# Optimization experiments

Measured on AMD Instinct MI355X. Metric: run time of the kernel, lower is better.

The kernel has to match this reference:

```python
import jax, jax.numpy as jnp
import numpy as np

EMBED_DIM = 1024
NUM_HEADS = 16
HEAD_DIM = EMBED_DIM // NUM_HEADS


def setup_inputs() -> dict:
    key = jax.random.key(0)
    k1, k2, k3, k4 = jax.random.split(key, 4)
    B, S, D = 2, 2048, EMBED_DIM
    x = jax.random.normal(k1, (B, S, D), dtype=jnp.float32)
    xpos = jax.random.randint(k2, (B, S), 0, 2048, dtype=jnp.int32)
    # torch nn.Linear weights: [out_features, in_features]; qkv_bias=False -> no qkv bias
    qkv_w = jax.random.normal(k3, (3 * D, D), dtype=jnp.float32) * (D ** -0.5)
    proj_w = jax.random.normal(k4, (D, D), dtype=jnp.float32) * (D ** -0.5)
    proj_b = jnp.zeros((D,), dtype=jnp.float32)
    return {"x": x, "xpos": xpos, "qkv_w": qkv_w, "proj_w": proj_w, "proj_b": proj_b}


def reference(x, xpos, qkv_w, proj_w, proj_b):
    # rope is None, dropout rates are 0, so xpos is unused and dropout is identity.
    B, S, D = x.shape
    H, hd = NUM_HEADS, D // NUM_HEADS
    scale = hd ** -0.5

    qkv = x @ qkv_w.T                                   # [B, S, 3D]
    qkv = qkv.reshape(B, S, 3, H, hd)
    qkv = jnp.transpose(qkv, (0, 3, 2, 1, 4))           # [B, H, 3, S, hd]
    q, k, v = qkv[:, :, 0], qkv[:, :, 1], qkv[:, :, 2]  # each [B, H, S, hd]

    scores = jnp.einsum("bhqd,bhkd->bhqk", q, k) * scale  # [B, H, S, S]
    probs = jax.nn.softmax(scores, axis=-1)
    out = jnp.einsum("bhqk,bhkd->bhqd", probs, v)         # [B, H, S, hd]

    out = jnp.transpose(out, (0, 2, 1, 3)).reshape(B, S, D)
    out = out @ proj_w.T + proj_b
    return out
```

## Files before the change

kernel.cpp:

```cpp
#include <hip/hip_runtime.h>


typedef __bf16 bf16_8 __attribute__((ext_vector_type(8)));
typedef __bf16 bf16_4 __attribute__((ext_vector_type(4)));
typedef __bf16 bf16_2 __attribute__((ext_vector_type(2)));
typedef float floatx4 __attribute__((ext_vector_type(4)));

#define MFMA16 __builtin_amdgcn_mfma_f32_16x16x32_bf16
#define CSCALE 0.1803368801111204f
#define EXP2R  __builtin_amdgcn_exp2f

__device__ __forceinline__ void gld16(const __bf16* g, __bf16* l) {
    __builtin_amdgcn_global_load_lds(
        (const __attribute__((address_space(1))) void*)g,
        (__attribute__((address_space(3))) void*)l, 16, 0, 0);
}

__device__ __forceinline__ unsigned pk_bf16(float a, float b) {
    bf16_2 t;
    t[0] = (__bf16)a; t[1] = (__bf16)b;
    return __builtin_bit_cast(unsigned, t);
}

__global__ __launch_bounds__(256) void cvt_all(
    const float* __restrict__ x, const float* __restrict__ w1,
    const float* __restrict__ w2,
    __bf16* __restrict__ xb, __bf16* __restrict__ w1b, __bf16* __restrict__ w2b)
{
    const int i = blockIdx.x * 256 + threadIdx.x;
    const float* src; __bf16* dst; int off;
    if (i < (1 << 20))                  { src = x;  dst = xb;  off = i; }
    else if (i < (1 << 20) + 786432)    { src = w1; dst = w1b; off = i - (1 << 20); }
    else                                { src = w2; dst = w2b; off = i - (1 << 20) - 786432; }
    float4 v = ((const float4*)src)[off];
    bf16_4 o;
    o[0] = (__bf16)v.x; o[1] = (__bf16)v.y; o[2] = (__bf16)v.z; o[3] = (__bf16)v.w;
    ((bf16_4*)dst)[off] = o;
}

__global__ __launch_bounds__(512) void qkv_gemm(
    const __bf16* __restrict__ X, const __bf16* __restrict__ W,
    __bf16* __restrict__ q_ws, __bf16* __restrict__ k_ws, __bf16* __restrict__ vt_ws)
{
    __shared__ __align__(16) __bf16 S[2][2][128 * 64];

    const int tid = threadIdx.x, lane = tid & 63;
    const int half = tid >> 8, htid = tid & 255;
    const int wvh = (tid >> 6) & 3;
    const int quad = lane >> 4, l15 = lane & 15;
    const int wm = (wvh >> 1) * 64, wn = (wvh & 1) * 64;
    const int m0 = blockIdx.y * 128, n0 = blockIdx.x * 128;
    const int c = n0 >> 10;

    const __bf16* Abase;
    const __bf16* Bbase;
    if (c == 2) { Abase = X + (size_t)m0 * 1024; Bbase = W + (size_t)n0 * 1024; }
    else        { Abase = W + (size_t)n0 * 1024; Bbase = X + (size_t)m0 * 1024; }
    Abase += half * 512;
    Bbase += half * 512;

    __bf16* As = S[half][0];
    __bf16* Bs = S[half][1];
    floatx4 acc[4][4] = {};

    for (int k0 = 0; k0 < 512; k0 += 64) {
        __syncthreads();
#pragma unroll
        for (int it = 0; it < 4; ++it) {
            int cc = it * 256 + htid;
            int row = cc >> 3, kc = cc & 7;
            gld16(Abase + row * 1024 + k0 + ((kc ^ (row & 7)) * 8), &As[cc * 8]);
        }
#pragma unroll
        for (int it = 0; it < 4; ++it) {
            int cc = it * 256 + htid;
            int row = cc >> 3, kc = cc & 7;
            gld16(Bbase + row * 1024 + k0 + ((kc ^ (row & 7)) * 8), &Bs[cc * 8]);
        }
        __syncthreads();

#pragma unroll
        for (int ks = 0; ks < 2; ++ks) {
            bf16_8 af[4], bf[4];
#pragma unroll
            for (int mt = 0; mt < 4; ++mt) {
                int r = wm + mt * 16 + l15;
                af[mt] = *(const bf16_8*)&As[r * 64 + (((ks * 4 + quad) ^ (r & 7)) * 8)];
            }
#pragma unroll
            for (int nt = 0; nt < 4; ++nt) {
                int r = wn + nt * 16 + l15;
                bf[nt] = *(const bf16_8*)&Bs[r * 64 + (((ks * 4 + quad) ^ (r & 7)) * 8)];
            }
#pragma unroll
            for (int mt = 0; mt < 4; ++mt)
#pragma unroll
                for (int nt = 0; nt < 4; ++nt)
                    acc[mt][nt] = MFMA16(af[mt], bf[nt], acc[mt][nt], 0, 0, 0);
        }
    }

    __syncthreads();
    float* comb = (float*)S;
    if (half == 1) {
#pragma unroll
        for (int mt = 0; mt < 4; ++mt)
#pragma unroll
            for (int nt = 0; nt < 4; ++nt)
                *(floatx4*)&comb[((mt * 4 + nt) * 256 + htid) * 4] = acc[mt][nt];
    }
    __syncthreads();
    if (half != 0) return;

#pragma unroll
    for (int mt = 0; mt < 4; ++mt)
#pragma unroll
        for (int nt = 0; nt < 4; ++nt)
            acc[mt][nt] += *(const floatx4*)&comb[((mt * 4 + nt) * 256 + htid) * 4];

    if (c == 2) {
#pragma unroll
        for (int mt = 0; mt < 4; ++mt) {
            const int mbase = m0 + wm + mt * 16 + quad * 4;
            const int b = mbase >> 11, s = mbase & 2047;
#pragma unroll
            for (int nt = 0; nt < 4; ++nt) {
                const int n = n0 + wn + nt * 16 + l15;
                const int h = (n >> 6) & 15, d = n & 63;
                bf16_4 pk;
#pragma unroll
                for (int r = 0; r < 4; ++r) pk[r] = (__bf16)acc[mt][nt][r];
                *(bf16_4*)&vt_ws[((b * 16 + h) * 64 + d) * 2048 + s] = pk;
            }
        }
    } else {
        __bf16* dst = (c == 0) ? q_ws : k_ws;
        const float scale = (c == 1) ? CSCALE : 1.0f;
#pragma unroll
        for (int mt = 0; mt < 4; ++mt) {
            const int nn = n0 + wm + mt * 16 + quad * 4;
            const int h = (nn >> 6) & 15, d0 = nn & 63;
#pragma unroll
            for (int nt = 0; nt < 4; ++nt) {
                const int token = m0 + wn + nt * 16 + l15;
                const int b = token >> 11, s = token & 2047;
                bf16_4 pk;
#pragma unroll
                for (int r = 0; r < 4; ++r) pk[r] = (__bf16)(acc[mt][nt][r] * scale);
                *(bf16_4*)&dst[((b * 16 + h) * 2048 + s) * 64 + d0] = pk;
            }
        }
    }
}

__global__ __launch_bounds__(512) void attn_kernel(
    const __bf16* __restrict__ q_ws, const __bf16* __restrict__ k_ws,
    const __bf16* __restrict__ vt_ws, __bf16* __restrict__ attn_ws)
{
    __shared__ __align__(16) __bf16 Ks [2][64 * 64];
    __shared__ __align__(16) __bf16 Vts[2][64 * 64];
    __shared__ __align__(16) __bf16 Ps [8][2][16][72];

    const int tid = threadIdx.x, lane = tid & 63, w = tid >> 6;
    const int half = tid >> 8, htid = tid & 255, wh = w & 3;
    const int quad = lane >> 4, l15 = lane & 15;
    const int bh = blockIdx.x, qt = blockIdx.y;
    const int q0 = qt * 128;
    const int koff = half * 1024;

    const __bf16* qp  = q_ws  + (size_t)bh * (2048 * 64);
    const __bf16* kp  = k_ws  + (size_t)bh * (2048 * 64);
    const __bf16* vtp = vt_ws + (size_t)bh * (64 * 2048);

    const int srow = htid >> 3, skc = htid & 7;
    const int sw   = (skc ^ (srow & 7)) * 8;
    const __bf16* kb0 = kp  + (size_t)(koff + srow) * 64 + sw;
    const __bf16* kb1 = kp  + (size_t)(koff + srow + 32) * 64 + sw;
    const __bf16* vb0 = vtp + (size_t)srow * 2048 + koff + sw;
    const __bf16* vb1 = vtp + (size_t)(srow + 32) * 2048 + koff + sw;
    const int ldsoff = (srow * 8 + skc) * 8;

    bf16_8 qf[2][2];
#pragma unroll
    for (int qg = 0; qg < 2; ++qg) {
        const int qrow = q0 + wh * 32 + qg * 16 + l15;
        qf[qg][0] = *(const bf16_8*)&qp[qrow * 64 + quad * 8];
        qf[qg][1] = *(const bf16_8*)&qp[qrow * 64 + 32 + quad * 8];
    }

    bf16_8 ones;
#pragma unroll
    for (int j = 0; j < 8; ++j) ones[j] = (__bf16)1.0f;

    floatx4 oacc[2][4] = {};
    floatx4 lsum[2] = {};

#pragma unroll 1
    for (int kt = 0; kt < 16; ++kt) {
        const int ko = kt * 64;
        __syncthreads();
        gld16(kb0 + ko * 64, &Ks[half][ldsoff]);
        gld16(kb1 + ko * 64, &Ks[half][ldsoff + 2048]);
        gld16(vb0 + ko,      &Vts[half][ldsoff]);
        gld16(vb1 + ko,      &Vts[half][ldsoff + 2048]);
        __syncthreads();

        const __bf16* Kb = Ks[half];
        const __bf16* Vb = Vts[half];

        floatx4 sacc[2][4] = {};
#pragma unroll
        for (int ks = 0; ks < 2; ++ks)
#pragma unroll
            for (int kg = 0; kg < 4; ++kg) {
                int krow = kg * 16 + l15;
                bf16_8 kf = *(const bf16_8*)&Kb[krow * 64 + (((ks * 4 + quad) ^ (krow & 7)) * 8)];
                sacc[0][kg] = MFMA16(kf, qf[0][ks], sacc[0][kg], 0, 0, 0);
                sacc[1][kg] = MFMA16(kf, qf[1][ks], sacc[1][kg], 0, 0, 0);
            }

#pragma unroll
        for (int qg = 0; qg < 2; ++qg)
#pragma unroll
            for (int kg = 0; kg < 4; ++kg) {
                uint2 pk;
                pk.x = pk_bf16(EXP2R(sacc[qg][kg][0]), EXP2R(sacc[qg][kg][1]));
                pk.y = pk_bf16(EXP2R(sacc[qg][kg][2]), EXP2R(sacc[qg][kg][3]));
                *(uint2*)&Ps[w][qg][l15][kg * 16 + quad * 4] = pk;
            }
        __asm__ __volatile__("s_waitcnt lgkmcnt(0)" ::: "memory");

#pragma unroll
        for (int ks = 0; ks < 2; ++ks) {
            bf16_8 pf0 = *(const bf16_8*)&Ps[w][0][l15][ks * 32 + quad * 8];
            bf16_8 pf1 = *(const bf16_8*)&Ps[w][1][l15][ks * 32 + quad * 8];
            lsum[0] = MFMA16(ones, pf0, lsum[0], 0, 0, 0);
            lsum[1] = MFMA16(ones, pf1, lsum[1], 0, 0, 0);
#pragma unroll
            for (int dg = 0; dg < 4; ++dg) {
                int drow = dg * 16 + l15;
                bf16_8 vf = *(const bf16_8*)&Vb[drow * 64 + (((ks * 4 + quad) ^ (drow & 7)) * 8)];
                oacc[0][dg] = MFMA16(vf, pf0, oacc[0][dg], 0, 0, 0);
                oacc[1][dg] = MFMA16(vf, pf1, oacc[1][dg], 0, 0, 0);
            }
        }
    }

    __syncthreads();
    float* comb  = (float*)Ps;
    float* lcomb = comb + 128 * 68;
    if (half == 1) {
#pragma unroll
        for (int qg = 0; qg < 2; ++qg) {
            const int q = wh * 32 + qg * 16 + l15;
#pragma unroll
            for (int dg = 0; dg < 4; ++dg)
                *(floatx4*)&comb[q * 68 + dg * 16 + quad * 4] = oacc[qg][dg];
            if (quad == 0) lcomb[q] = lsum[qg][0];
        }
    }
    __syncthreads();
    if (half == 0) {
        const int b = bh >> 4, h = bh & 15;
#pragma unroll
        for (int qg = 0; qg < 2; ++qg) {
            const int q = wh * 32 + qg * 16 + l15;
            const float inv_l = 1.0f / (lsum[qg][0] + lcomb[q]);
            const int token = b * 2048 + q0 + q;
#pragma unroll
            for (int dg = 0; dg < 4; ++dg) {
                floatx4 v2 = *(const floatx4*)&comb[q * 68 + dg * 16 + quad * 4];
                bf16_4 ok;
#pragma unroll
                for (int r = 0; r < 4; ++r)
                    ok[r] = (__bf16)((oacc[qg][dg][r] + v2[r]) * inv_l);
                *(bf16_4*)&attn_ws[(size_t)token * 1024 + h * 64 + dg * 16 + quad * 4] = ok;
            }
        }
    }
}

__global__ __launch_bounds__(256) void proj_gemm(
    const __bf16* __restrict__ Ain, const __bf16* __restrict__ W,
    const float* __restrict__ bias, float* __restrict__ out)
{
    __shared__ __align__(16) __bf16 As[128 * 64];
    __shared__ __align__(16) __bf16 Bs[64 * 64];
    floatx4 acc[4][2] = {};
    const int m0 = blockIdx.y * 128, n0 = blockIdx.x * 64;

    const int tid = threadIdx.x, lane = tid & 63, wv = tid >> 6;
    const int quad = lane >> 4, l15 = lane & 15;
    const int wm = (wv >> 1) * 64, wn = (wv & 1) * 32;

    const __bf16* A  = Ain + (size_t)m0 * 1024;
    const __bf16* Bp = W   + (size_t)n0 * 1024;

    for (int k0 = 0; k0 < 1024; k0 += 64) {
        __syncthreads();
#pragma unroll
        for (int it = 0; it < 4; ++it) {
            int cc = it * 256 + tid;
            int row = cc >> 3, kc = cc & 7;
            gld16(A + row * 1024 + k0 + ((kc ^ (row & 7)) * 8), &As[cc * 8]);
        }
#pragma unroll
        for (int it = 0; it < 2; ++it) {
            int cc = it * 256 + tid;
            int row = cc >> 3, kc = cc & 7;
            gld16(Bp + row * 1024 + k0 + ((kc ^ (row & 7)) * 8), &Bs[cc * 8]);
        }
        __syncthreads();

#pragma unroll
        for (int ks = 0; ks < 2; ++ks) {
            bf16_8 af[4], bf[2];
#pragma unroll
            for (int mt = 0; mt < 4; ++mt) {
                int r = wm + mt * 16 + l15;
                af[mt] = *(const bf16_8*)&As[r * 64 + (((ks * 4 + quad) ^ (r & 7)) * 8)];
            }
#pragma unroll
            for (int nt = 0; nt < 2; ++nt) {
                int r = wn + nt * 16 + l15;
                bf[nt] = *(const bf16_8*)&Bs[r * 64 + (((ks * 4 + quad) ^ (r & 7)) * 8)];
            }
#pragma unroll
            for (int mt = 0; mt < 4; ++mt)
#pragma unroll
                for (int nt = 0; nt < 2; ++nt)
                    acc[mt][nt] = MFMA16(af[mt], bf[nt], acc[mt][nt], 0, 0, 0);
        }
    }

    float bv[2];
#pragma unroll
    for (int nt = 0; nt < 2; ++nt) bv[nt] = bias[n0 + wn + nt * 16 + l15];

#pragma unroll
    for (int mt = 0; mt < 4; ++mt) {
        const int m = m0 + wm + mt * 16 + quad * 4;
#pragma unroll
        for (int nt = 0; nt < 2; ++nt) {
            const int n = n0 + wn + nt * 16 + l15;
#pragma unroll
            for (int r = 0; r < 4; ++r)
                out[(size_t)(m + r) * 1024 + n] = acc[mt][nt][r] + bv[nt];
        }
    }
}

extern "C" void kernel_launch(void* const* d_in, const int* in_sizes, int n_in,
                              void* d_out, int out_size, void* d_ws, size_t ws_size,
                              hipStream_t stream)
{
    const float* x      = (const float*)d_in[0];
    const float* qkv_w  = (const float*)d_in[2];
    const float* proj_w = (const float*)d_in[3];
    const float* proj_b = (const float*)d_in[4];
    float* out = (float*)d_out;

    const size_t SZ   = 4096 * 1024;
    const size_t WQKV = 3072 * 1024;
    const size_t WPRJ = 1024 * 1024;

    __bf16* xb      = (__bf16*)d_ws;
    __bf16* qkvwb   = xb + SZ;
    __bf16* projwb  = qkvwb + WQKV;
    __bf16* q_ws    = projwb + WPRJ;
    __bf16* k_ws    = q_ws + SZ;
    __bf16* vt_ws   = k_ws + SZ;
    __bf16* attn_ws = vt_ws + SZ;

    cvt_all<<<dim3(8192), 256, 0, stream>>>(x, qkv_w, proj_w, xb, qkvwb, projwb);
    qkv_gemm  <<<dim3(24, 32), 512, 0, stream>>>(xb, qkvwb, q_ws, k_ws, vt_ws);
    attn_kernel<<<dim3(32, 16), 512, 0, stream>>>(q_ws, k_ws, vt_ws, attn_ws);
    proj_gemm <<<dim3(16, 32), 256, 0, stream>>>(attn_ws, projwb, proj_b, out);
}
```

Measured before the change: 180.6 us.

## Double-buffer K/V and projection tiles; drop split-K attention halves

The attention kernel no longer splits the key range across two half-blocks of 256 threads, each holding 2 query groups. Now all 8 waves share one 64-key tile per step, each wave owns 16 query rows, and the loop runs 32 steps. K/V tiles are double-buffered so the next tile's global-to-LDS load overlaps the current MFMA work, and s_setprio raises priority around the MFMA sections. The final cross-half LDS combine is removed. The projection GEMM gets the same double-buffered LDS prefetch, doubling its shared memory. The trade-offs are less per-wave work to hide latency, more LDS use and possibly lower occupancy in proj_gemm.

New measurement: 183.9 us. Within noise of the previous version (+1.8%).

```diff
diff --git a/kernel.cpp b/kernel.cpp
--- a/kernel.cpp
+++ b/kernel.cpp
@@ -159,124 +159,119 @@
 {
     __shared__ __align__(16) __bf16 Ks [2][64 * 64];
     __shared__ __align__(16) __bf16 Vts[2][64 * 64];
-    __shared__ __align__(16) __bf16 Ps [8][2][16][72];
+    __shared__ __align__(16) __bf16 Ps [8][16][72];
 
     const int tid = threadIdx.x, lane = tid & 63, w = tid >> 6;
-    const int half = tid >> 8, htid = tid & 255, wh = w & 3;
     const int quad = lane >> 4, l15 = lane & 15;
     const int bh = blockIdx.x, qt = blockIdx.y;
     const int q0 = qt * 128;
-    const int koff = half * 1024;
 
     const __bf16* qp  = q_ws  + (size_t)bh * (2048 * 64);
     const __bf16* kp  = k_ws  + (size_t)bh * (2048 * 64);
     const __bf16* vtp = vt_ws + (size_t)bh * (64 * 2048);
 
-    const int srow = htid >> 3, skc = htid & 7;
+    const int srow = tid >> 3, skc = tid & 7;
     const int sw   = (skc ^ (srow & 7)) * 8;
-    const __bf16* kb0 = kp  + (size_t)(koff + srow) * 64 + sw;
-    const __bf16* kb1 = kp  + (size_t)(koff + srow + 32) * 64 + sw;
-    const __bf16* vb0 = vtp + (size_t)srow * 2048 + koff + sw;
-    const __bf16* vb1 = vtp + (size_t)(srow + 32) * 2048 + koff + sw;
-    const int ldsoff = (srow * 8 + skc) * 8;
-
-    bf16_8 qf[2][2];
-#pragma unroll
-    for (int qg = 0; qg < 2; ++qg) {
-        const int qrow = q0 + wh * 32 + qg * 16 + l15;
-        qf[qg][0] = *(const bf16_8*)&qp[qrow * 64 + quad * 8];
-        qf[qg][1] = *(const bf16_8*)&qp[qrow * 64 + 32 + quad * 8];
+    const __bf16* kb = kp  + (size_t)srow * 64 + sw;
+    const __bf16* vb = vtp + (size_t)srow * 2048 + sw;
+    const int ldsoff = tid * 8;
+
+    bf16_8 qf[2];
+    {
+        const int qrow = q0 + w * 16 + l15;
+        qf[0] = *(const bf16_8*)&qp[qrow * 64 + quad * 8];
+        qf[1] = *(const bf16_8*)&qp[qrow * 64 + 32 + quad * 8];
     }
 
     bf16_8 ones;
 #pragma unroll
     for (int j = 0; j < 8; ++j) ones[j] = (__bf16)1.0f;
 
-    floatx4 oacc[2][4] = {};
-    floatx4 lsum[2] = {};
-
-#pragma unroll 1
-    for (int kt = 0; kt < 16; ++kt) {
-        const int ko = kt * 64;
-        __syncthreads();
-        gld16(kb0 + ko * 64, &Ks[half][ldsoff]);
-        gld16(kb1 + ko * 64, &Ks[half][ldsoff + 2048]);
-        gld16(vb0 + ko,      &Vts[half][ldsoff]);
-        gld16(vb1 + ko,      &Vts[half][ldsoff + 2048]);
-        __syncthreads();
-
-        const __bf16* Kb = Ks[half];
-        const __bf16* Vb = Vts[half];
-
-        floatx4 sacc[2][4] = {};
+    floatx4 oacc[4] = {};
+    floatx4 lsum = {};
+
+    gld16(kb, &Ks[0][ldsoff]);
+    gld16(vb, &Vts[0][ldsoff]);
+    __syncthreads();
+
+#pragma unroll 2
+    for (int kt = 0; kt < 32; ++kt) {
+        const int cur = kt & 1;
+        if (kt < 31) {
+            gld16(kb + (size_t)(kt + 1) * 4096, &Ks[cur ^ 1][ldsoff]);
+            gld16(vb + (size_t)(kt + 1) * 64,   &Vts[cur ^ 1][ldsoff]);
+        }
+        const __bf16* Kb = Ks[cur];
+        const __bf16* Vb = Vts[cur];
+
+        floatx4 sacc[4] = {};
+        __builtin_amdgcn_s_setprio(1);
 #pragma unroll
         for (int ks = 0; ks < 2; ++ks)
 #pragma unroll
             for (int kg = 0; kg < 4; ++kg) {
-                int krow = kg * 16 + l15;
+                const int krow = kg * 16 + l15;
                 bf16_8 kf = *(const bf16_8*)&Kb[krow * 64 + (((ks * 4 + quad) ^ (krow & 7)) * 8)];
-                sacc[0][kg] = MFMA16(kf, qf[0][ks], sacc[0][kg], 0, 0, 0);
-                sacc[1][kg] = MFMA16(kf, qf[1][ks], sacc[1][kg], 0, 0, 0);
-            }
-
-#pragma unroll
-        for (int qg = 0; qg < 2; ++qg)
-#pragma unroll
-            for (int kg = 0; kg < 4; ++kg) {
-                uint2 pk;
-                pk.x = pk_bf16(EXP2R(sacc[qg][kg][0]), EXP2R(sacc[qg][kg][1]));
-                pk.y = pk_bf16(EXP2R(sacc[qg][kg][2]), EXP2R(sacc[qg][kg][3]));
-                *(uint2*)&Ps[w][qg][l15][kg * 16 + quad * 4] = pk;
-            }
+                sacc[kg] = MFMA16(kf, qf[ks], sacc[kg], 0, 0, 0);
+            }
+        __builtin_amdgcn_s_setprio(0);
+
+#pragma unroll
+        for (int kg = 0; kg < 4; ++kg) {
+            uint2 pk;
+            pk.x = pk_bf16(EXP2R(sacc[kg][0]), EXP2R(sacc[kg][1]));
+            pk.y = pk_bf16(EXP2R(sacc[kg][2]), EXP2R(sacc[kg][3]));
+            *(uint2*)&Ps[w][l15][kg * 16 + quad * 4] = pk;
+        }
         __asm__ __volatile__("s_waitcnt lgkmcnt(0)" ::: "memory");
 
+        __builtin_amdgcn_s_setprio(1);
 #pragma unroll
         for (int ks = 0; ks < 2; ++ks) {
-            bf16_8 pf0 = *(const bf16_8*)&Ps[w][0][l15][ks * 32 + quad * 8];
-            bf16_8 pf1 = *(const bf16_8*)&Ps[w][1][l15][ks * 32 + quad * 8];
-            lsum[0] = MFMA16(ones, pf0, lsum[0], 0, 0, 0);
-            lsum[1] = MFMA16(ones, pf1, lsum[1], 0, 0, 0);
+            bf16_8 pf = *(const bf16_8*)&Ps[w][l15][ks * 32 + quad * 8];
+            lsum = MFMA16(ones, pf, lsum, 0, 0, 0);
 #pragma unroll
             for (int dg = 0; dg < 4; ++dg) {
-                int drow = dg * 16 + l15;
+                const int drow = dg * 16 + l15;
                 bf16_8 vf = *(const bf16_8*)&Vb[drow * 64 + (((ks * 4 + quad) ^ (drow & 7)) * 8)];
-                oacc[0][dg] = MFMA16(vf, pf0, oacc[0][dg], 0, 0, 0);
-                oacc[1][dg] = MFMA16(vf, pf1, oacc[1][dg], 0, 0, 0);
-            }
-        }
-    }
-
-    __syncthreads();
-    float* comb  = (float*)Ps;
-    float* lcomb = comb + 128 * 68;
-    if (half == 1) {
-#pragma unroll
-        for (int qg = 0; qg < 2; ++qg) {
-            const int q = wh * 32 + qg * 16 + l15;
-#pragma unroll
-            for (int dg = 0; dg < 4; ++dg)
-                *(floatx4*)&comb[q * 68 + dg * 16 + quad * 4] = oacc[qg][dg];
-            if (quad == 0) lcomb[q] = lsum[qg][0];
-        }
-    }
-    __syncthreads();
-    if (half == 0) {
-        const int b = bh >> 4, h = bh & 15;
-#pragma unroll
-        for (int qg = 0; qg < 2; ++qg) {
-            const int q = wh * 32 + qg * 16 + l15;
-            const float inv_l = 1.0f / (lsum[qg][0] + lcomb[q]);
-            const int token = b * 2048 + q0 + q;
-#pragma unroll
-            for (int dg = 0; dg < 4; ++dg) {
-                floatx4 v2 = *(const floatx4*)&comb[q * 68 + dg * 16 + quad * 4];
-                bf16_4 ok;
-#pragma unroll
-                for (int r = 0; r < 4; ++r)
-                    ok[r] = (__bf16)((oacc[qg][dg][r] + v2[r]) * inv_l);
-                *(bf16_4*)&attn_ws[(size_t)token * 1024 + h * 64 + dg * 16 + quad * 4] = ok;
-            }
-        }
+                oacc[dg] = MFMA16(vf, pf, oacc[dg], 0, 0, 0);
+            }
+        }
+        __builtin_amdgcn_s_setprio(0);
+
+        if (kt < 31) {
+            __asm__ __volatile__("s_waitcnt vmcnt(0)" ::: "memory");
+            __syncthreads();
+        }
+    }
+
+    const int b = bh >> 4, h = bh & 15;
+    const float inv_l = 1.0f / lsum[0];
+    const int token = b * 2048 + q0 + w * 16 + l15;
+#pragma unroll
+    for (int dg = 0; dg < 4; ++dg) {
+        bf16_4 ok;
+#pragma unroll
+        for (int r = 0; r < 4; ++r) ok[r] = (__bf16)(oacc[dg][r] * inv_l);
+        *(bf16_4*)&attn_ws[(size_t)token * 1024 + h * 64 + dg * 16 + quad * 4] = ok;
+    }
+}
+
+__device__ __forceinline__ void proj_stage(
+    const __bf16* __restrict__ A, const __bf16* __restrict__ Bp,
+    int k0, __bf16* As, __bf16* Bs, int tid)
+{
+#pragma unroll
+    for (int it = 0; it < 4; ++it) {
+        int cc = it * 256 + tid;
+        int row = cc >> 3, kc = cc & 7;
+        gld16(A + row * 1024 + k0 + ((kc ^ (row & 7)) * 8), &As[cc * 8]);
+    }
+#pragma unroll
+    for (int it = 0; it < 2; ++it) {
+        int cc = it * 256 + tid;
+        int row = cc >> 3, kc = cc & 7;
+        gld16(Bp + row * 1024 + k0 + ((kc ^ (row & 7)) * 8), &Bs[cc * 8]);
     }
 }
 
@@ -284,8 +279,8 @@
     const __bf16* __restrict__ Ain, const __bf16* __restrict__ W,
     const float* __restrict__ bias, float* __restrict__ out)
 {
-    __shared__ __align__(16) __bf16 As[128 * 64];
-    __shared__ __align__(16) __bf16 Bs[64 * 64];
+    __shared__ __align__(16) __bf16 As[2][128 * 64];
+    __shared__ __align__(16) __bf16 Bs[2][64 * 64];
     floatx4 acc[4][2] = {};
     const int m0 = blockIdx.y * 128, n0 = blockIdx.x * 64;
 
@@ -296,40 +291,40 @@
     const __bf16* A  = Ain + (size_t)m0 * 1024;
     const __bf16* Bp = W   + (size_t)n0 * 1024;
 
-    for (int k0 = 0; k0 < 1024; k0 += 64) {
-        __syncthreads();
-#pragma unroll
-        for (int it = 0; it < 4; ++it) {
-            int cc = it * 256 + tid;
-            int row = cc >> 3, kc = cc & 7;
-            gld16(A + row * 1024 + k0 + ((kc ^ (row & 7)) * 8), &As[cc * 8]);
-        }
-#pragma unroll
-        for (int it = 0; it < 2; ++it) {
-            int cc = it * 256 + tid;
-            int row = cc >> 3, kc = cc & 7;
-            gld16(Bp + row * 1024 + k0 + ((kc ^ (row & 7)) * 8), &Bs[cc * 8]);
-        }
-        __syncthreads();
-
+    proj_stage(A, Bp, 0, As[0], Bs[0], tid);
+    __syncthreads();
+
+#pragma unroll 2
+    for (int kk = 0; kk < 16; ++kk) {
+        const int cur = kk & 1;
+        if (kk < 15)
+            proj_stage(A, Bp, (kk + 1) * 64, As[cur ^ 1], Bs[cur ^ 1], tid);
+
+        const __bf16* Ab = As[cur];
+        const __bf16* Bb = Bs[cur];
 #pragma unroll
         for (int ks = 0; ks < 2; ++ks) {
             bf16_8 af[4], bf[2];
 #pragma unroll
             for (int mt = 0; mt < 4; ++mt) {
                 int r = wm + mt * 16 + l15;
-                af[mt] = *(const bf16_8*)&As[r * 64 + (((ks * 4 + quad) ^ (r & 7)) * 8)];
+                af[mt] = *(const bf16_8*)&Ab[r * 64 + (((ks * 4 + quad) ^ (r & 7)) * 8)];
             }
 #pragma unroll
             for (int nt = 0; nt < 2; ++nt) {
                 int r = wn + nt * 16 + l15;
-                bf[nt] = *(const bf16_8*)&Bs[r * 64 + (((ks * 4 + quad) ^ (r & 7)) * 8)];
+                bf[nt] = *(const bf16_8*)&Bb[r * 64 + (((ks * 4 + quad) ^ (r & 7)) * 8)];
             }
 #pragma unroll
             for (int mt = 0; mt < 4; ++mt)
 #pragma unroll
                 for (int nt = 0; nt < 2; ++nt)
                     acc[mt][nt] = MFMA16(af[mt], bf[nt], acc[mt][nt], 0, 0, 0);
+        }
+
+        if (kk < 15) {
+            __asm__ __volatile__("s_waitcnt vmcnt(0)" ::: "memory");
+            __syncthreads();
         }
     }
 
```
